# Performance work log

Measured on AMD Instinct MI355X. Metric: run time of the kernel, lower is better.

The kernel has to match this reference:

```python
import jax, jax.numpy as jnp
import numpy as np

B, T, D = 64, 2048, 300

def setup_inputs() -> dict:
    key = jax.random.key(0)
    k1, k2, k3, k4 = jax.random.split(key, 4)
    gate_encoding = jax.random.uniform(k1, (B, T, D), dtype=jnp.float32)
    inputs_encoding = jax.random.normal(k2, (B, T, D), dtype=jnp.float32)
    # kaiming-normal-ish init: std = sqrt(2 / fan_in)
    std = float(np.sqrt(2.0 / D))
    Wz = jax.random.normal(k3, (D, D), dtype=jnp.float32) * std
    Wo = jax.random.normal(k4, (D, D), dtype=jnp.float32) * std
    bz = jnp.zeros((D,), dtype=jnp.float32)
    bo = jnp.zeros((D,), dtype=jnp.float32)
    return {"gate_encoding": gate_encoding, "inputs_encoding": inputs_encoding,
            "Wz": Wz, "bz": bz, "Wo": Wo, "bo": bo}

def reference(gate_encoding, inputs_encoding, Wz, bz, Wo, bo):
    # Batch the two linear projections across all timesteps (torch.nn.Linear: x @ W.T + b)
    z = jnp.tanh(jnp.einsum('btd,ed->bte', inputs_encoding, Wz) + bz)  # [B,T,D]
    o = jnp.tanh(jnp.einsum('btd,ed->bte', inputs_encoding, Wo) + bo)  # [B,T,D]

    # Sequential gated recurrence: c_t = g_t * c_{t-1} + (1 - g_t) * z_t ; h_t = o_t * c_t
    def step(c, gz_o):
        g_t, z_t, o_t = gz_o
        c = g_t * c + (1.0 - g_t) * z_t
        return c, o_t * c

    c0 = jnp.zeros((gate_encoding.shape[0], gate_encoding.shape[2]), dtype=inputs_encoding.dtype)
    # scan over time: move T to leading axis
    _, h = jax.lax.scan(step, c0,
                        (jnp.swapaxes(gate_encoding, 0, 1),
                         jnp.swapaxes(z, 0, 1),
                         jnp.swapaxes(o, 0, 1)))
    return jnp.swapaxes(h, 0, 1)  # [B,T,D]
```

## Files before the change

### kernel.cpp

```cpp
#include <hip/hip_runtime.h>
#include <hip/hip_bf16.h>

typedef _Float16 f16x8 __attribute__((ext_vector_type(8)));
typedef float f32x4 __attribute__((ext_vector_type(4)));

#define B_SZ 64
#define T_SZ 2048
#define D_SZ 300
#define M_SZ (B_SZ * T_SZ)
#define KP 320
#define NP 640
#define NCHUNK 16
#define CLEN 128

__device__ __forceinline__ void gld_lds16(const void* g, void* l) {
    __builtin_amdgcn_global_load_lds(
        (const __attribute__((address_space(1))) unsigned int*)g,
        (__attribute__((address_space(3))) unsigned int*)l,
        16, 0, 0);
}

__device__ __forceinline__ float fast_tanh(float x) {
    float e = __expf(2.0f * x);
    return 1.0f - 2.0f * __builtin_amdgcn_rcpf(e + 1.0f);
}

__global__ void pack_x(const float* __restrict__ in, _Float16* __restrict__ out) {
    unsigned int i = blockIdx.x * 256u + threadIdx.x;
    unsigned int row = i / KP;
    unsigned int k = i - row * KP;
    float v = (k < D_SZ) ? in[(size_t)row * D_SZ + k] : 0.0f;
    out[i] = (_Float16)v;
}

__global__ void pack_w(const float* __restrict__ Wz, const float* __restrict__ Wo,
                       _Float16* __restrict__ W) {
    unsigned int i = blockIdx.x * 256u + threadIdx.x;
    if (i >= NP * KP) return;
    unsigned int n = i / KP;
    unsigned int k = i - n * KP;
    float v = 0.0f;
    if (k < D_SZ) {
        if (n < D_SZ) v = Wz[n * D_SZ + k];
        else if (n >= 320 && n < 320 + D_SZ) v = Wo[(n - 320) * D_SZ + k];
    }
    W[i] = (_Float16)v;
}

__global__ void pack_bias(const float* __restrict__ bz, const float* __restrict__ bo,
                          float* __restrict__ bias) {
    int n = threadIdx.x;
    float v = 0.0f;
    if (n < D_SZ) v = bz[n];
    else if (n >= 320 && n < 320 + D_SZ) v = bo[n - 320];
    bias[n] = v;
}

__global__ __launch_bounds__(256) void gemm_zo(const _Float16* __restrict__ X,
                                               const _Float16* __restrict__ W,
                                               const float* __restrict__ bias,
                                               _Float16* __restrict__ C) {
    __shared__ _Float16 As[2][128 * 32];
    __shared__ _Float16 Bs[2][128 * 32];

    const int tid = threadIdx.x;
    const int lane = tid & 63;
    const int wid = tid >> 6;
    const int wm = wid >> 1, wn = wid & 1;

    int g = blockIdx.x;
    int s = (g & 7) * (5120 / 8) + (g >> 3);
    int bm = s / 5;
    int bn = s - bm * 5;

    f32x4 acc[4][4] = {};

    const int r_in_c = lane >> 2;
    const int u_phys = lane & 3;

    auto stage = [&](int buf, int kt) {
#pragma unroll
        for (int j = 0; j < 2; ++j) {
            int c = wid + j * 4;
            int row = c * 16 + r_in_c;
            int ul = u_phys ^ ((row >> 1) & 3);
            const _Float16* ga = X + ((size_t)(bm * 128 + row) * KP + kt * 32 + ul * 8);
            gld_lds16(ga, &As[buf][c * 512]);
            const _Float16* gb = W + ((size_t)(bn * 128 + row) * KP + kt * 32 + ul * 8);
            gld_lds16(gb, &Bs[buf][c * 512]);
        }
    };

    stage(0, 0);
    __syncthreads();

    int buf = 0;
#pragma unroll 1
    for (int kt = 0; kt < 10; ++kt) {
        if (kt < 9) stage(buf ^ 1, kt + 1);

        f16x8 af[4], bf[4];
#pragma unroll
        for (int ms = 0; ms < 4; ++ms) {
            int row = wm * 64 + ms * 16 + (lane & 15);
            int u = (lane >> 4) ^ ((row >> 1) & 3);
            af[ms] = *(const f16x8*)&As[buf][row * 32 + u * 8];
        }
#pragma unroll
        for (int ns = 0; ns < 4; ++ns) {
            int row = wn * 64 + ns * 16 + (lane & 15);
            int u = (lane >> 4) ^ ((row >> 1) & 3);
            bf[ns] = *(const f16x8*)&Bs[buf][row * 32 + u * 8];
        }
#pragma unroll
        for (int ms = 0; ms < 4; ++ms)
#pragma unroll
            for (int ns = 0; ns < 4; ++ns)
                acc[ms][ns] = __builtin_amdgcn_mfma_f32_16x16x32_f16(af[ms], bf[ns], acc[ms][ns], 0, 0, 0);

        __syncthreads();
        buf ^= 1;
    }

    const int mrow0 = bm * 128 + wm * 64;
    const int ncol0 = bn * 128 + wn * 64;
#pragma unroll
    for (int ns = 0; ns < 4; ++ns) {
        int n = ncol0 + ns * 16 + (lane & 15);
        float bv = bias[n];
#pragma unroll
        for (int ms = 0; ms < 4; ++ms) {
            int m0 = mrow0 + ms * 16 + (lane >> 4) * 4;
#pragma unroll
            for (int r = 0; r < 4; ++r) {
                float v = fast_tanh(acc[ms][ns][r] + bv);
                C[(size_t)(m0 + r) * NP + n] = (_Float16)v;
            }
        }
    }
}

__global__ void scan_p1(const float* __restrict__ gate, const _Float16* __restrict__ C,
                        float* __restrict__ Aout, float* __restrict__ Bout) {
    int b = blockIdx.x >> 4;
    int nc = blockIdx.x & 15;
    int d = threadIdx.x;
    if (d >= D_SZ) return;
    size_t base = (size_t)b * T_SZ + (size_t)nc * CLEN;
    const float* gp = gate + base * D_SZ + d;
    const _Float16* zp = C + base * NP + d;
    float A = 1.0f, Bc = 0.0f;
    for (int t = 0; t < CLEN; ++t) {
        float gv = gp[(size_t)t * D_SZ];
        float zv = (float)zp[(size_t)t * NP];
        A *= gv;
        Bc = gv * Bc + (1.0f - gv) * zv;
    }
    int o = (b * NCHUNK + nc) * D_SZ + d;
    Aout[o] = A;
    Bout[o] = Bc;
}

__global__ void scan_p2(const float* __restrict__ A, const float* __restrict__ Bc,
                        float* __restrict__ Cin) {
    int idx = blockIdx.x * 256 + threadIdx.x;
    if (idx >= B_SZ * D_SZ) return;
    int b = idx / D_SZ;
    int d = idx - b * D_SZ;
    float c = 0.0f;
    for (int nc = 0; nc < NCHUNK; ++nc) {
        int o = (b * NCHUNK + nc) * D_SZ + d;
        Cin[o] = c;
        c = A[o] * c + Bc[o];
    }
}

__global__ void scan_p3(const float* __restrict__ gate, const _Float16* __restrict__ C,
                        const float* __restrict__ Cin, float* __restrict__ out) {
    int b = blockIdx.x >> 4;
    int nc = blockIdx.x & 15;
    int d = threadIdx.x;
    if (d >= D_SZ) return;
    size_t base = (size_t)b * T_SZ + (size_t)nc * CLEN;
    const float* gp = gate + base * D_SZ + d;
    const _Float16* zp = C + base * NP + d;
    const _Float16* op = zp + 320;
    float* hp = out + base * D_SZ + d;
    float c = Cin[(b * NCHUNK + nc) * D_SZ + d];
    for (int t = 0; t < CLEN; ++t) {
        float gv = gp[(size_t)t * D_SZ];
        float zv = (float)zp[(size_t)t * NP];
        float ov = (float)op[(size_t)t * NP];
        c = gv * c + (1.0f - gv) * zv;
        hp[(size_t)t * D_SZ] = ov * c;
    }
}

extern "C" void kernel_launch(void* const* d_in, const int* in_sizes, int n_in,
                              void* d_out, int out_size, void* d_ws, size_t ws_size,
                              hipStream_t stream) {
    const float* gate = (const float*)d_in[0];
    const float* xin  = (const float*)d_in[1];
    const float* Wz   = (const float*)d_in[2];
    const float* bz   = (const float*)d_in[3];
    const float* Wo   = (const float*)d_in[4];
    const float* bo   = (const float*)d_in[5];
    float* out = (float*)d_out;

    char* ws = (char*)d_ws;
    _Float16* Xf16 = (_Float16*)(ws);
    _Float16* C16  = (_Float16*)(ws + 83886080ull);
    _Float16* Wc   = (_Float16*)(ws + 251658240ull);
    float*    bias = (float*)   (ws + 252067840ull);
    float*    Ach  = (float*)   (ws + 252070400ull);
    float*    Bch  = (float*)   (ws + 253299200ull);
    float*    Cin  = (float*)   (ws + 254528000ull);

    pack_x<<<(M_SZ * KP) / 256, 256, 0, stream>>>(xin, Xf16);
    pack_w<<<(NP * KP + 255) / 256, 256, 0, stream>>>(Wz, Wo, Wc);
    pack_bias<<<1, NP, 0, stream>>>(bz, bo, bias);

    gemm_zo<<<(M_SZ / 128) * (NP / 128), 256, 0, stream>>>(Xf16, Wc, bias, C16);

    scan_p1<<<B_SZ * NCHUNK, 320, 0, stream>>>(gate, C16, Ach, Bch);
    scan_p2<<<(B_SZ * D_SZ + 255) / 256, 256, 0, stream>>>(Ach, Bch, Cin);
    scan_p3<<<B_SZ * NCHUNK, 320, 0, stream>>>(gate, C16, Cin, out);
}
```

Baseline: 343.4 us.

## Enlarge GEMM tile, vectorize packing and epilogue stores, double scan chunks

The GEMM block grows to 256x128 with 512 threads, so each W tile loaded into LDS is reused across more rows. The MFMA operands are swapped so each lane holds four consecutive output columns, which lets the epilogue write f16x4 vectors. pack_x now reads float4 from the input and a separate pad_x kernel zero-fills the padding columns. The scan is split into 32 chunks of 64 steps for more parallelism, and the chunk buffers move into the start of the workspace, reusing the Xf16 region after the GEMM has consumed it. The costs are an extra kernel launch, more LDS per block, and scattered 2-byte stores in pack_x.

```diff
diff --git a/kernel.cpp b/kernel.cpp
--- a/kernel.cpp
+++ b/kernel.cpp
@@ -2,6 +2,7 @@
 #include <hip/hip_bf16.h>
 
 typedef _Float16 f16x8 __attribute__((ext_vector_type(8)));
+typedef _Float16 f16x4 __attribute__((ext_vector_type(4)));
 typedef float f32x4 __attribute__((ext_vector_type(4)));
 
 #define B_SZ 64
@@ -10,8 +11,8 @@
 #define M_SZ (B_SZ * T_SZ)
 #define KP 320
 #define NP 640
-#define NCHUNK 16
-#define CLEN 128
+#define NCHUNK 32
+#define CLEN 64
 
 __device__ __forceinline__ void gld_lds16(const void* g, void* l) {
     __builtin_amdgcn_global_load_lds(
@@ -27,10 +28,23 @@
 
 __global__ void pack_x(const float* __restrict__ in, _Float16* __restrict__ out) {
     unsigned int i = blockIdx.x * 256u + threadIdx.x;
-    unsigned int row = i / KP;
-    unsigned int k = i - row * KP;
-    float v = (k < D_SZ) ? in[(size_t)row * D_SZ + k] : 0.0f;
-    out[i] = (_Float16)v;
+    f32x4 v = *(const f32x4*)(in + (size_t)i * 4);
+#pragma unroll
+    for (int j = 0; j < 4; ++j) {
+        unsigned int f = i * 4 + j;
+        unsigned int row = f / D_SZ;
+        unsigned int k = f - row * D_SZ;
+        out[(size_t)row * KP + k] = (_Float16)v[j];
+    }
+}
+
+__global__ void pad_x(_Float16* __restrict__ out) {
+    unsigned int i = blockIdx.x * 256u + threadIdx.x;
+    unsigned int j = i * 4;
+    unsigned int row = j / 20;
+    unsigned int k0 = j - row * 20;
+    f16x4 z = {};
+    *(f16x4*)(out + (size_t)row * KP + 300 + k0) = z;
 }
 
 __global__ void pack_w(const float* __restrict__ Wz, const float* __restrict__ Wo,
@@ -56,11 +70,11 @@
     bias[n] = v;
 }
 
-__global__ __launch_bounds__(256) void gemm_zo(const _Float16* __restrict__ X,
+__global__ __launch_bounds__(512) void gemm_zo(const _Float16* __restrict__ X,
                                                const _Float16* __restrict__ W,
                                                const float* __restrict__ bias,
                                                _Float16* __restrict__ C) {
-    __shared__ _Float16 As[2][128 * 32];
+    __shared__ _Float16 As[2][256 * 32];
     __shared__ _Float16 Bs[2][128 * 32];
 
     const int tid = threadIdx.x;
@@ -69,7 +83,7 @@
     const int wm = wid >> 1, wn = wid & 1;
 
     int g = blockIdx.x;
-    int s = (g & 7) * (5120 / 8) + (g >> 3);
+    int s = (g & 7) * (2560 / 8) + (g >> 3);
     int bm = s / 5;
     int bn = s - bm * 5;
 
@@ -81,11 +95,16 @@
     auto stage = [&](int buf, int kt) {
 #pragma unroll
         for (int j = 0; j < 2; ++j) {
-            int c = wid + j * 4;
+            int c = wid + j * 8;
             int row = c * 16 + r_in_c;
             int ul = u_phys ^ ((row >> 1) & 3);
-            const _Float16* ga = X + ((size_t)(bm * 128 + row) * KP + kt * 32 + ul * 8);
+            const _Float16* ga = X + ((size_t)(bm * 256 + row) * KP + kt * 32 + ul * 8);
             gld_lds16(ga, &As[buf][c * 512]);
+        }
+        {
+            int c = wid;
+            int row = c * 16 + r_in_c;
+            int ul = u_phys ^ ((row >> 1) & 3);
             const _Float16* gb = W + ((size_t)(bn * 128 + row) * KP + kt * 32 + ul * 8);
             gld_lds16(gb, &Bs[buf][c * 512]);
         }
@@ -99,13 +118,7 @@
     for (int kt = 0; kt < 10; ++kt) {
         if (kt < 9) stage(buf ^ 1, kt + 1);
 
-        f16x8 af[4], bf[4];
-#pragma unroll
-        for (int ms = 0; ms < 4; ++ms) {
-            int row = wm * 64 + ms * 16 + (lane & 15);
-            int u = (lane >> 4) ^ ((row >> 1) & 3);
-            af[ms] = *(const f16x8*)&As[buf][row * 32 + u * 8];
-        }
+        f16x8 bf[4];
 #pragma unroll
         for (int ns = 0; ns < 4; ++ns) {
             int row = wn * 64 + ns * 16 + (lane & 15);
@@ -113,37 +126,41 @@
             bf[ns] = *(const f16x8*)&Bs[buf][row * 32 + u * 8];
         }
 #pragma unroll
-        for (int ms = 0; ms < 4; ++ms)
+        for (int ms = 0; ms < 4; ++ms) {
+            int row = wm * 64 + ms * 16 + (lane & 15);
+            int u = (lane >> 4) ^ ((row >> 1) & 3);
+            f16x8 af = *(const f16x8*)&As[buf][row * 32 + u * 8];
 #pragma unroll
             for (int ns = 0; ns < 4; ++ns)
-                acc[ms][ns] = __builtin_amdgcn_mfma_f32_16x16x32_f16(af[ms], bf[ns], acc[ms][ns], 0, 0, 0);
+                acc[ms][ns] = __builtin_amdgcn_mfma_f32_16x16x32_f16(bf[ns], af, acc[ms][ns], 0, 0, 0);
+        }
 
         __syncthreads();
         buf ^= 1;
     }
 
-    const int mrow0 = bm * 128 + wm * 64;
+    const int mrow0 = bm * 256 + wm * 64;
     const int ncol0 = bn * 128 + wn * 64;
 #pragma unroll
     for (int ns = 0; ns < 4; ++ns) {
-        int n = ncol0 + ns * 16 + (lane & 15);
-        float bv = bias[n];
+        int nb = ncol0 + ns * 16 + (lane >> 4) * 4;
+        f32x4 b4 = *(const f32x4*)&bias[nb];
 #pragma unroll
         for (int ms = 0; ms < 4; ++ms) {
-            int m0 = mrow0 + ms * 16 + (lane >> 4) * 4;
-#pragma unroll
-            for (int r = 0; r < 4; ++r) {
-                float v = fast_tanh(acc[ms][ns][r] + bv);
-                C[(size_t)(m0 + r) * NP + n] = (_Float16)v;
-            }
+            int m = mrow0 + ms * 16 + (lane & 15);
+            f16x4 v;
+#pragma unroll
+            for (int r = 0; r < 4; ++r)
+                v[r] = (_Float16)fast_tanh(acc[ms][ns][r] + b4[r]);
+            *(f16x4*)&C[(size_t)m * NP + nb] = v;
         }
     }
 }
 
 __global__ void scan_p1(const float* __restrict__ gate, const _Float16* __restrict__ C,
                         float* __restrict__ Aout, float* __restrict__ Bout) {
-    int b = blockIdx.x >> 4;
-    int nc = blockIdx.x & 15;
+    int b = blockIdx.x >> 5;
+    int nc = blockIdx.x & 31;
     int d = threadIdx.x;
     if (d >= D_SZ) return;
     size_t base = (size_t)b * T_SZ + (size_t)nc * CLEN;
@@ -177,8 +194,8 @@
 
 __global__ void scan_p3(const float* __restrict__ gate, const _Float16* __restrict__ C,
                         const float* __restrict__ Cin, float* __restrict__ out) {
-    int b = blockIdx.x >> 4;
-    int nc = blockIdx.x & 15;
+    int b = blockIdx.x >> 5;
+    int nc = blockIdx.x & 31;
     int d = threadIdx.x;
     if (d >= D_SZ) return;
     size_t base = (size_t)b * T_SZ + (size_t)nc * CLEN;
@@ -212,15 +229,16 @@
     _Float16* C16  = (_Float16*)(ws + 83886080ull);
     _Float16* Wc   = (_Float16*)(ws + 251658240ull);
     float*    bias = (float*)   (ws + 252067840ull);
-    float*    Ach  = (float*)   (ws + 252070400ull);
-    float*    Bch  = (float*)   (ws + 253299200ull);
-    float*    Cin  = (float*)   (ws + 254528000ull);
-
-    pack_x<<<(M_SZ * KP) / 256, 256, 0, stream>>>(xin, Xf16);
+    float*    Ach  = (float*)   (ws);
+    float*    Bch  = (float*)   (ws + 2457600ull);
+    float*    Cin  = (float*)   (ws + 4915200ull);
+
+    pack_x<<<(M_SZ * D_SZ / 4) / 256, 256, 0, stream>>>(xin, Xf16);
+    pad_x<<<(M_SZ * 20 / 4) / 256, 256, 0, stream>>>(Xf16);
     pack_w<<<(NP * KP + 255) / 256, 256, 0, stream>>>(Wz, Wo, Wc);
     pack_bias<<<1, NP, 0, stream>>>(bz, bo, bias);
 
-    gemm_zo<<<(M_SZ / 128) * (NP / 128), 256, 0, stream>>>(Xf16, Wc, bias, C16);
+    gemm_zo<<<(M_SZ / 256) * (NP / 128), 512, 0, stream>>>(Xf16, Wc, bias, C16);
 
     scan_p1<<<B_SZ * NCHUNK, 320, 0, stream>>>(gate, C16, Ach, Bch);
     scan_p2<<<(B_SZ * D_SZ + 255) / 256, 256, 0, stream>>>(Ach, Bch, Cin);
```

After: 328.4 us. -4.4%, faster.
